# Performance work log

Hardware: AMD Instinct MI355X
Metric: run time of the kernel (lower is better)

The kernel has to match this reference:

```python
import jax, jax.numpy as jnp
import numpy as np

NEG_SLOPE = 0.1  # LeakyReLU alpha from __init__
EPS = 1e-5


def setup_inputs() -> dict:
    key = jax.random.key(0)
    k1, k2, k3, k4, k5 = jax.random.split(key, 5)
    N, E, DIN, DOUT = 10000, 160000, 1024, 1024
    x = jax.random.normal(k1, (N, DIN), dtype=jnp.float32)
    W = jax.random.normal(k2, (DIN, DOUT), dtype=jnp.float32) * 0.02  # xavier-ish gain
    a = jax.random.normal(k3, (1, 2 * DOUT), dtype=jnp.float32) * 0.02
    src = jax.random.randint(k4, (E,), 0, N, dtype=jnp.int64)  # edge rows i
    dst = jax.random.randint(k5, (E,), 0, N, dtype=jnp.int64)  # edge cols j
    return {"x": x, "W": W, "a": a, "src": src, "dst": dst}


def reference(x, W, a, src, dst):
    N = x.shape[0]
    d = W.shape[1]
    h = x @ W                                   # [N, d]
    # a @ cat(h_src, h_dst)^T == (h @ a_l)[src] + (h @ a_r)[dst]
    a_l, a_r = a[0, :d], a[0, d:]
    al = h @ a_l                                # [N]
    ar = h @ a_r                                # [N]
    e = jnp.exp(-jax.nn.leaky_relu(al[src] + ar[dst], negative_slope=NEG_SLOPE))  # [E]
    # sparse rowsum: A @ ones  ->  segment_sum of e over rows
    rowsum = jax.ops.segment_sum(e, src, num_segments=N)          # [N]
    # sparse aggregate: A @ h  (dropout = identity in eval mode)
    h_prime = jax.ops.segment_sum(e[:, None] * h[dst], src, num_segments=N)  # [N, d]
    h_prime = h_prime / (rowsum[:, None] + EPS)
    return jax.nn.elu(h_prime)  # concat=True branch
```

## Files before the change

### kernel.cpp

```cpp
#include <hip/hip_runtime.h>
#include <hip/hip_bf16.h>
#include <stdint.h>
#include <math.h>

#define DK 1024
#define DN 1024
#define CAP 64

typedef __attribute__((ext_vector_type(8))) short bf16x8;
typedef __attribute__((ext_vector_type(4))) float f32x4;

__device__ __forceinline__ unsigned short f2bf(float f) {
  union { float f; uint32_t u; } v; v.f = f;
  uint32_t r = v.u + 0x7FFFu + ((v.u >> 16) & 1u);
  return (unsigned short)(r >> 16);
}
__device__ __forceinline__ float bf2f(unsigned short b) {
  union { uint32_t u; float f; } v; v.u = ((uint32_t)b) << 16; return v.f;
}

__device__ __forceinline__ void gload_lds16(const void* g, void* l) {
  __builtin_amdgcn_global_load_lds((const __attribute__((address_space(1))) unsigned int*)g,
                                   (__attribute__((address_space(3))) unsigned int*)l,
                                   16, 0, 0);
}

__device__ __forceinline__ void block_reduce2(float& pl, float& pr) {
#pragma unroll
  for (int off = 32; off >= 1; off >>= 1) {
    pl += __shfl_down(pl, off);
    pr += __shfl_down(pr, off);
  }
  __shared__ float sl[4], sr[4];
  int w = threadIdx.x >> 6, lane = threadIdx.x & 63;
  if (lane == 0) { sl[w] = pl; sr[w] = pr; }
  __syncthreads();
  if (threadIdx.x == 0) {
    pl = sl[0] + sl[1] + sl[2] + sl[3];
    pr = sr[0] + sr[1] + sr[2] + sr[3];
  }
}

__global__ __launch_bounds__(256) void wvec_kernel(const float* __restrict__ W,
                                                   const float* __restrict__ a,
                                                   float* __restrict__ wl,
                                                   float* __restrict__ wr,
                                                   int* __restrict__ cnt, int M) {
  int idx = blockIdx.x * 256 + threadIdx.x;
  if (idx < M) cnt[idx] = 0;
  int k = blockIdx.x;
  int tid = threadIdx.x;
  float4 wv = ((const float4*)(W + (size_t)k * DN))[tid];
  float4 l4 = ((const float4*)a)[tid];
  float4 r4 = ((const float4*)(a + DN))[tid];
  float pl = wv.x * l4.x + wv.y * l4.y + wv.z * l4.z + wv.w * l4.w;
  float pr = wv.x * r4.x + wv.y * r4.y + wv.z * r4.z + wv.w * r4.w;
  block_reduce2(pl, pr);
  if (tid == 0) { wl[k] = pl; wr[k] = pr; }
}

__global__ __launch_bounds__(256) void prep_kernel(const float* __restrict__ x,
                                                   unsigned short* __restrict__ xb,
                                                   const float* __restrict__ W,
                                                   unsigned short* __restrict__ Wt,
                                                   const float* __restrict__ wl,
                                                   const float* __restrict__ wr,
                                                   float* __restrict__ al,
                                                   float* __restrict__ ar,
                                                   int M) {
  if ((int)blockIdx.x < M) {
    int row = blockIdx.x;
    int tid = threadIdx.x;
    float4 v = ((const float4*)(x + (size_t)row * DK))[tid];
    ushort4 o;
    o.x = f2bf(v.x); o.y = f2bf(v.y); o.z = f2bf(v.z); o.w = f2bf(v.w);
    ((ushort4*)(xb + (size_t)row * DK))[tid] = o;
    float4 l4 = ((const float4*)wl)[tid];
    float4 r4 = ((const float4*)wr)[tid];
    float pl = v.x * l4.x + v.y * l4.y + v.z * l4.z + v.w * l4.w;
    float pr = v.x * r4.x + v.y * r4.y + v.z * r4.z + v.w * r4.w;
    block_reduce2(pl, pr);
    if (tid == 0) { al[row] = pl; ar[row] = pr; }
  } else {
    __shared__ float t[32][33];
    int bid = blockIdx.x - M;
    int tx = threadIdx.x & 31, ty = threadIdx.x >> 5;
    int bk = (bid & 31) * 32, bn = (bid >> 5) * 32;
#pragma unroll
    for (int rr = 0; rr < 4; ++rr) {
      int row = ty + rr * 8;
      t[row][tx] = W[(size_t)(bk + row) * DN + bn + tx];
    }
    __syncthreads();
#pragma unroll
    for (int rr = 0; rr < 4; ++rr) {
      int row = ty + rr * 8;
      Wt[(size_t)(bn + row) * DK + bk + tx] = f2bf(t[tx][row]);
    }
  }
}

__global__ __launch_bounds__(256) void gemm_kernel(const unsigned short* __restrict__ A,
                                                   const unsigned short* __restrict__ Bt,
                                                   unsigned short* __restrict__ Hb,
                                                   int M) {
  __shared__ unsigned short As[128 * 32];
  __shared__ unsigned short Bs[128 * 32];
  const int tid = threadIdx.x;
  const int w = tid >> 6, lane = tid & 63;
  const int r = lane & 15, q = lane >> 4;
  const int m0 = blockIdx.x * 128, n0 = blockIdx.y * 128;
  const int wr = (w >> 1) * 64, wc = (w & 1) * 64;

  const int c0 = w * 64 + lane;
  const int rowA0 = c0 >> 2, g0 = c0 & 3;
  const int rowA1 = rowA0 + 64;
  int gr0 = m0 + rowA0; if (gr0 >= M) gr0 = M - 1;
  int gr1 = m0 + rowA1; if (gr1 >= M) gr1 = M - 1;
  const unsigned short* gA0 = A + (size_t)gr0 * DK + g0 * 8;
  const unsigned short* gA1 = A + (size_t)gr1 * DK + g0 * 8;
  const unsigned short* gB0 = Bt + (size_t)(n0 + rowA0) * DK + g0 * 8;
  const unsigned short* gB1 = Bt + (size_t)(n0 + rowA1) * DK + g0 * 8;
  unsigned short* lA0 = As + w * 512;
  unsigned short* lA1 = As + 2048 + w * 512;
  unsigned short* lB0 = Bs + w * 512;
  unsigned short* lB1 = Bs + 2048 + w * 512;

  const f32x4 zero = {0.f, 0.f, 0.f, 0.f};
  f32x4 acc[4][4];
#pragma unroll
  for (int i = 0; i < 4; ++i)
#pragma unroll
    for (int j = 0; j < 4; ++j) acc[i][j] = zero;

  for (int k0 = 0; k0 < DK; k0 += 32) {
    gload_lds16(gA0, lA0);
    gload_lds16(gA1, lA1);
    gload_lds16(gB0, lB0);
    gload_lds16(gB1, lB1);
    gA0 += 32; gA1 += 32; gB0 += 32; gB1 += 32;
    __syncthreads();

    bf16x8 af[4], bfr[4];
#pragma unroll
    for (int i = 0; i < 4; ++i)
      af[i] = *(const bf16x8*)&As[(wr + i * 16 + r) * 32 + q * 8];
#pragma unroll
    for (int j = 0; j < 4; ++j)
      bfr[j] = *(const bf16x8*)&Bs[(wc + j * 16 + r) * 32 + q * 8];
#pragma unroll
    for (int i = 0; i < 4; ++i)
#pragma unroll
      for (int j = 0; j < 4; ++j)
        acc[i][j] = __builtin_amdgcn_mfma_f32_16x16x32_bf16(af[i], bfr[j], acc[i][j], 0, 0, 0);
    __syncthreads();
  }

#pragma unroll
  for (int i = 0; i < 4; ++i) {
#pragma unroll
    for (int reg = 0; reg < 4; ++reg) {
      int m = m0 + wr + i * 16 + q * 4 + reg;
      if (m < M) {
#pragma unroll
        for (int j = 0; j < 4; ++j) {
          int n = n0 + wc + j * 16 + r;
          Hb[(size_t)m * DN + n] = f2bf(acc[i][j][reg]);
        }
      }
    }
  }
}

__global__ __launch_bounds__(256) void edge_kernel(const int* __restrict__ src,
                                                   const int* __restrict__ dst,
                                                   const float* __restrict__ al,
                                                   const float* __restrict__ ar,
                                                   int* __restrict__ cnt,
                                                   int* __restrict__ bdst,
                                                   float* __restrict__ be, int E) {
  int i = blockIdx.x * 256 + threadIdx.x;
  if (i < E) {
    int s = src[i], d = dst[i];
    float v = al[s] + ar[d];
    float lr = v > 0.f ? v : 0.1f * v;
    float e = expf(-lr);
    int pos = atomicAdd(&cnt[s], 1);
    if (pos < CAP) {
      bdst[(s << 6) + pos] = d;
      be[(s << 6) + pos] = e;
    }
  }
}

__global__ __launch_bounds__(256) void aggregate_kernel(const int* __restrict__ cnt,
                                                        const int* __restrict__ bdst,
                                                        const float* __restrict__ be,
                                                        const unsigned short* __restrict__ Hb,
                                                        float* __restrict__ out, int M) {
  int row = blockIdx.x;
  int tid = threadIdx.x;
  int n = cnt[row]; if (n > CAP) n = CAP;
  int base = row << 6;
  size_t coff = (size_t)tid * 4;
  float a0 = 0.f, a1 = 0.f, a2 = 0.f, a3 = 0.f, rs = 0.f;
  int p = 0;
  for (; p + 8 <= n; p += 8) {
    int4 da = *(const int4*)(bdst + base + p);
    int4 db = *(const int4*)(bdst + base + p + 4);
    float4 ea = *(const float4*)(be + base + p);
    float4 eb = *(const float4*)(be + base + p + 4);
    ushort4 h0 = *(const ushort4*)&Hb[(size_t)da.x * DN + coff];
    ushort4 h1 = *(const ushort4*)&Hb[(size_t)da.y * DN + coff];
    ushort4 h2 = *(const ushort4*)&Hb[(size_t)da.z * DN + coff];
    ushort4 h3 = *(const ushort4*)&Hb[(size_t)da.w * DN + coff];
    ushort4 h4 = *(const ushort4*)&Hb[(size_t)db.x * DN + coff];
    ushort4 h5 = *(const ushort4*)&Hb[(size_t)db.y * DN + coff];
    ushort4 h6 = *(const ushort4*)&Hb[(size_t)db.z * DN + coff];
    ushort4 h7 = *(const ushort4*)&Hb[(size_t)db.w * DN + coff];
    rs += ((ea.x + ea.y) + (ea.z + ea.w)) + ((eb.x + eb.y) + (eb.z + eb.w));
    a0 += ea.x * bf2f(h0.x) + ea.y * bf2f(h1.x) + ea.z * bf2f(h2.x) + ea.w * bf2f(h3.x)
        + eb.x * bf2f(h4.x) + eb.y * bf2f(h5.x) + eb.z * bf2f(h6.x) + eb.w * bf2f(h7.x);
    a1 += ea.x * bf2f(h0.y) + ea.y * bf2f(h1.y) + ea.z * bf2f(h2.y) + ea.w * bf2f(h3.y)
        + eb.x * bf2f(h4.y) + eb.y * bf2f(h5.y) + eb.z * bf2f(h6.y) + eb.w * bf2f(h7.y);
    a2 += ea.x * bf2f(h0.z) + ea.y * bf2f(h1.z) + ea.z * bf2f(h2.z) + ea.w * bf2f(h3.z)
        + eb.x * bf2f(h4.z) + eb.y * bf2f(h5.z) + eb.z * bf2f(h6.z) + eb.w * bf2f(h7.z);
    a3 += ea.x * bf2f(h0.w) + ea.y * bf2f(h1.w) + ea.z * bf2f(h2.w) + ea.w * bf2f(h3.w)
        + eb.x * bf2f(h4.w) + eb.y * bf2f(h5.w) + eb.z * bf2f(h6.w) + eb.w * bf2f(h7.w);
  }
  for (; p + 4 <= n; p += 4) {
    int4 d4 = *(const int4*)(bdst + base + p);
    float4 e4 = *(const float4*)(be + base + p);
    ushort4 h0 = *(const ushort4*)&Hb[(size_t)d4.x * DN + coff];
    ushort4 h1 = *(const ushort4*)&Hb[(size_t)d4.y * DN + coff];
    ushort4 h2 = *(const ushort4*)&Hb[(size_t)d4.z * DN + coff];
    ushort4 h3 = *(const ushort4*)&Hb[(size_t)d4.w * DN + coff];
    rs += (e4.x + e4.y) + (e4.z + e4.w);
    a0 += e4.x * bf2f(h0.x) + e4.y * bf2f(h1.x) + e4.z * bf2f(h2.x) + e4.w * bf2f(h3.x);
    a1 += e4.x * bf2f(h0.y) + e4.y * bf2f(h1.y) + e4.z * bf2f(h2.y) + e4.w * bf2f(h3.y);
    a2 += e4.x * bf2f(h0.z) + e4.y * bf2f(h1.z) + e4.z * bf2f(h2.z) + e4.w * bf2f(h3.z);
    a3 += e4.x * bf2f(h0.w) + e4.y * bf2f(h1.w) + e4.z * bf2f(h2.w) + e4.w * bf2f(h3.w);
  }
  for (; p < n; ++p) {
    int d = bdst[base + p];
    float e = be[base + p];
    rs += e;
    ushort4 hv = *(const ushort4*)&Hb[(size_t)d * DN + coff];
    a0 += e * bf2f(hv.x);
    a1 += e * bf2f(hv.y);
    a2 += e * bf2f(hv.z);
    a3 += e * bf2f(hv.w);
  }
  float inv = 1.f / (rs + 1e-5f);
  float4 o; float v;
  v = a0 * inv; o.x = v > 0.f ? v : (expf(v) - 1.f);
  v = a1 * inv; o.y = v > 0.f ? v : (expf(v) - 1.f);
  v = a2 * inv; o.z = v > 0.f ? v : (expf(v) - 1.f);
  v = a3 * inv; o.w = v > 0.f ? v : (expf(v) - 1.f);
  ((float4*)(out + (size_t)row * DN))[tid] = o;
}

extern "C" void kernel_launch(void* const* d_in, const int* in_sizes, int n_in,
                              void* d_out, int out_size, void* d_ws, size_t ws_size,
                              hipStream_t stream) {
  const float* x = (const float*)d_in[0];
  const float* W = (const float*)d_in[1];
  const float* a = (const float*)d_in[2];
  const int* src = (const int*)d_in[3];
  const int* dst = (const int*)d_in[4];
  float* out = (float*)d_out;
  const int M = in_sizes[0] / DK;
  const int E = in_sizes[3];

  size_t off = 0;
  auto alloc = [&](size_t bytes) -> void* {
    void* p = (char*)d_ws + off;
    off += (bytes + 255) & ~(size_t)255;
    return p;
  };
  unsigned short* xb   = (unsigned short*)alloc((size_t)M * DK * 2);
  unsigned short* Wt   = (unsigned short*)alloc((size_t)DK * DN * 2);
  unsigned short* Hb   = (unsigned short*)alloc((size_t)M * DN * 2);
  float*          al   = (float*)alloc((size_t)M * 4);
  float*          ar   = (float*)alloc((size_t)M * 4);
  float*          wl   = (float*)alloc((size_t)DK * 4);
  float*          wr   = (float*)alloc((size_t)DK * 4);
  int*            cnt  = (int*)alloc((size_t)M * 4);
  int*            bdst = (int*)alloc((size_t)M * CAP * 4);
  float*          be   = (float*)alloc((size_t)M * CAP * 4);

  wvec_kernel<<<DK, 256, 0, stream>>>(W, a, wl, wr, cnt, M);
  prep_kernel<<<M + (DK / 32) * (DN / 32), 256, 0, stream>>>(x, xb, W, Wt, wl, wr, al, ar, M);
  gemm_kernel<<<dim3((M + 127) / 128, DN / 128), 256, 0, stream>>>(xb, Wt, Hb, M);
  edge_kernel<<<(E + 255) / 256, 256, 0, stream>>>(src, dst, al, ar, cnt, bdst, be, E);
  aggregate_kernel<<<M, 256, 0, stream>>>(cnt, bdst, be, Hb, out, M);
}
```

Before: 194.7 us.

## Shrink GEMM M-tile to 64 rows and XOR-swizzle LDS tiles

Changes the GEMM block tile from 128x128 to 64x128, so each wave computes a 32x64 sub-tile and twice as many blocks launch. This gives more blocks for the 256 CUs (the 10000x1024 output previously made only ~632 blocks). It also applies an XOR swizzle on the 16-byte chunk index in the LDS tiles to reduce bank conflicts on fragment reads. The cost is less data reuse per block, with the B tile loaded twice as often from global memory.

Result: slower. 200.7 us (+3.1%).

```diff
diff --git a/kernel.cpp b/kernel.cpp
--- a/kernel.cpp
+++ b/kernel.cpp
@@ -104,52 +104,55 @@
                                                    const unsigned short* __restrict__ Bt,
                                                    unsigned short* __restrict__ Hb,
                                                    int M) {
-  __shared__ unsigned short As[128 * 32];
+  __shared__ unsigned short As[64 * 32];
   __shared__ unsigned short Bs[128 * 32];
   const int tid = threadIdx.x;
   const int w = tid >> 6, lane = tid & 63;
   const int r = lane & 15, q = lane >> 4;
-  const int m0 = blockIdx.x * 128, n0 = blockIdx.y * 128;
-  const int wr = (w >> 1) * 64, wc = (w & 1) * 64;
-
-  const int c0 = w * 64 + lane;
-  const int rowA0 = c0 >> 2, g0 = c0 & 3;
-  const int rowA1 = rowA0 + 64;
-  int gr0 = m0 + rowA0; if (gr0 >= M) gr0 = M - 1;
-  int gr1 = m0 + rowA1; if (gr1 >= M) gr1 = M - 1;
-  const unsigned short* gA0 = A + (size_t)gr0 * DK + g0 * 8;
-  const unsigned short* gA1 = A + (size_t)gr1 * DK + g0 * 8;
-  const unsigned short* gB0 = Bt + (size_t)(n0 + rowA0) * DK + g0 * 8;
-  const unsigned short* gB1 = Bt + (size_t)(n0 + rowA1) * DK + g0 * 8;
-  unsigned short* lA0 = As + w * 512;
-  unsigned short* lA1 = As + 2048 + w * 512;
-  unsigned short* lB0 = Bs + w * 512;
-  unsigned short* lB1 = Bs + 2048 + w * 512;
+  const int m0 = blockIdx.x * 64, n0 = blockIdx.y * 128;
+  const int wr = (w >> 1) * 32, wc = (w & 1) * 64;
+
+  const int cA = w * 64 + lane;
+  const int rA = cA >> 2, gA = (cA & 3) ^ ((rA >> 1) & 3);
+  int grA = m0 + rA; if (grA >= M) grA = M - 1;
+  const unsigned short* gpA = A + (size_t)grA * DK + gA * 8;
+  unsigned short* lpA = As + w * 512;
+
+  const int cB0 = w * 64 + lane, cB1 = cB0 + 256;
+  const int rB0 = cB0 >> 2, gB0i = (cB0 & 3) ^ ((rB0 >> 1) & 3);
+  const int rB1 = cB1 >> 2, gB1i = (cB1 & 3) ^ ((rB1 >> 1) & 3);
+  const unsigned short* gpB0 = Bt + (size_t)(n0 + rB0) * DK + gB0i * 8;
+  const unsigned short* gpB1 = Bt + (size_t)(n0 + rB1) * DK + gB1i * 8;
+  unsigned short* lpB0 = Bs + w * 512;
+  unsigned short* lpB1 = Bs + 2048 + w * 512;
 
   const f32x4 zero = {0.f, 0.f, 0.f, 0.f};
-  f32x4 acc[4][4];
-#pragma unroll
-  for (int i = 0; i < 4; ++i)
+  f32x4 acc[2][4];
+#pragma unroll
+  for (int i = 0; i < 2; ++i)
 #pragma unroll
     for (int j = 0; j < 4; ++j) acc[i][j] = zero;
 
   for (int k0 = 0; k0 < DK; k0 += 32) {
-    gload_lds16(gA0, lA0);
-    gload_lds16(gA1, lA1);
-    gload_lds16(gB0, lB0);
-    gload_lds16(gB1, lB1);
-    gA0 += 32; gA1 += 32; gB0 += 32; gB1 += 32;
+    gload_lds16(gpA, lpA);
+    gload_lds16(gpB0, lpB0);
+    gload_lds16(gpB1, lpB1);
+    gpA += 32; gpB0 += 32; gpB1 += 32;
     __syncthreads();
 
-    bf16x8 af[4], bfr[4];
-#pragma unroll
-    for (int i = 0; i < 4; ++i)
-      af[i] = *(const bf16x8*)&As[(wr + i * 16 + r) * 32 + q * 8];
-#pragma unroll
-    for (int j = 0; j < 4; ++j)
-      bfr[j] = *(const bf16x8*)&Bs[(wc + j * 16 + r) * 32 + q * 8];
-#pragma unroll
-    for (int i = 0; i < 4; ++i)
+    bf16x8 af[2], bfr[4];
+#pragma unroll
+    for (int i = 0; i < 2; ++i) {
+      int rr = wr + i * 16 + r;
+      af[i] = *(const bf16x8*)&As[rr * 32 + ((q ^ ((rr >> 1) & 3)) * 8)];
+    }
+#pragma unroll
+    for (int j = 0; j < 4; ++j) {
+      int rn = wc + j * 16 + r;
+      bfr[j] = *(const bf16x8*)&Bs[rn * 32 + ((q ^ ((rn >> 1) & 3)) * 8)];
+    }
+#pragma unroll
+    for (int i = 0; i < 2; ++i)
 #pragma unroll
       for (int j = 0; j < 4; ++j)
         acc[i][j] = __builtin_amdgcn_mfma_f32_16x16x32_bf16(af[i], bfr[j], acc[i][j], 0, 0, 0);
@@ -157,7 +160,7 @@
   }
 
 #pragma unroll
-  for (int i = 0; i < 4; ++i) {
+  for (int i = 0; i < 2; ++i) {
 #pragma unroll
     for (int reg = 0; reg < 4; ++reg) {
       int m = m0 + wr + i * 16 + q * 4 + reg;
@@ -291,7 +294,7 @@
 
   wvec_kernel<<<DK, 256, 0, stream>>>(W, a, wl, wr, cnt, M);
   prep_kernel<<<M + (DK / 32) * (DN / 32), 256, 0, stream>>>(x, xb, W, Wt, wl, wr, al, ar, M);
-  gemm_kernel<<<dim3((M + 127) / 128, DN / 128), 256, 0, stream>>>(xb, Wt, Hb, M);
+  gemm_kernel<<<dim3((M + 63) / 64, DN / 128), 256, 0, stream>>>(xb, Wt, Hb, M);
   edge_kernel<<<(E + 255) / 256, 256, 0, stream>>>(src, dst, al, ar, cnt, bdst, be, E);
   aggregate_kernel<<<M, 256, 0, stream>>>(cnt, bdst, be, Hb, out, M);
 }
```

## Split aggregate over column chunks with one wave per row

Applied to the files above, without the earlier changes.

The aggregate kernel now gives each wave one row and one 128-column chunk, and the grid covers 8 column chunks by row groups of 4. Chunks are ordered outermost, so concurrently running blocks all touch the same 128-column slice of H. This aims to keep the gathered H slice resident in L2/MALL instead of streaming full 2KB rows. In exchange each lane issues narrower 4-byte gathers, the 8-way unrolled loop is dropped, and the bdst/be index lists are re-read once per chunk.

New measurement: 200.7 us. 3.1% more time.

```diff
diff --git a/kernel.cpp b/kernel.cpp
--- a/kernel.cpp
+++ b/kernel.cpp
@@ -6,6 +6,7 @@
 #define DK 1024
 #define DN 1024
 #define CAP 64
+#define NCHUNK 8
 
 typedef __attribute__((ext_vector_type(8))) short bf16x8;
 typedef __attribute__((ext_vector_type(4))) float f32x4;
@@ -197,67 +198,43 @@
                                                         const int* __restrict__ bdst,
                                                         const float* __restrict__ be,
                                                         const unsigned short* __restrict__ Hb,
-                                                        float* __restrict__ out, int M) {
-  int row = blockIdx.x;
-  int tid = threadIdx.x;
+                                                        float* __restrict__ out,
+                                                        int M, int nrowgrp) {
+  int chunk = blockIdx.x / nrowgrp;
+  int rowgrp = blockIdx.x - chunk * nrowgrp;
+  int wv = threadIdx.x >> 6, lane = threadIdx.x & 63;
+  int row = rowgrp * 4 + wv;
+  if (row >= M) return;
   int n = cnt[row]; if (n > CAP) n = CAP;
   int base = row << 6;
-  size_t coff = (size_t)tid * 4;
-  float a0 = 0.f, a1 = 0.f, a2 = 0.f, a3 = 0.f, rs = 0.f;
+  int col = chunk * 128 + lane * 2;
+  const unsigned short* hb = Hb + col;
+  float a0 = 0.f, a1 = 0.f, rs = 0.f;
   int p = 0;
-  for (; p + 8 <= n; p += 8) {
-    int4 da = *(const int4*)(bdst + base + p);
-    int4 db = *(const int4*)(bdst + base + p + 4);
-    float4 ea = *(const float4*)(be + base + p);
-    float4 eb = *(const float4*)(be + base + p + 4);
-    ushort4 h0 = *(const ushort4*)&Hb[(size_t)da.x * DN + coff];
-    ushort4 h1 = *(const ushort4*)&Hb[(size_t)da.y * DN + coff];
-    ushort4 h2 = *(const ushort4*)&Hb[(size_t)da.z * DN + coff];
-    ushort4 h3 = *(const ushort4*)&Hb[(size_t)da.w * DN + coff];
-    ushort4 h4 = *(const ushort4*)&Hb[(size_t)db.x * DN + coff];
-    ushort4 h5 = *(const ushort4*)&Hb[(size_t)db.y * DN + coff];
-    ushort4 h6 = *(const ushort4*)&Hb[(size_t)db.z * DN + coff];
-    ushort4 h7 = *(const ushort4*)&Hb[(size_t)db.w * DN + coff];
-    rs += ((ea.x + ea.y) + (ea.z + ea.w)) + ((eb.x + eb.y) + (eb.z + eb.w));
-    a0 += ea.x * bf2f(h0.x) + ea.y * bf2f(h1.x) + ea.z * bf2f(h2.x) + ea.w * bf2f(h3.x)
-        + eb.x * bf2f(h4.x) + eb.y * bf2f(h5.x) + eb.z * bf2f(h6.x) + eb.w * bf2f(h7.x);
-    a1 += ea.x * bf2f(h0.y) + ea.y * bf2f(h1.y) + ea.z * bf2f(h2.y) + ea.w * bf2f(h3.y)
-        + eb.x * bf2f(h4.y) + eb.y * bf2f(h5.y) + eb.z * bf2f(h6.y) + eb.w * bf2f(h7.y);
-    a2 += ea.x * bf2f(h0.z) + ea.y * bf2f(h1.z) + ea.z * bf2f(h2.z) + ea.w * bf2f(h3.z)
-        + eb.x * bf2f(h4.z) + eb.y * bf2f(h5.z) + eb.z * bf2f(h6.z) + eb.w * bf2f(h7.z);
-    a3 += ea.x * bf2f(h0.w) + ea.y * bf2f(h1.w) + ea.z * bf2f(h2.w) + ea.w * bf2f(h3.w)
-        + eb.x * bf2f(h4.w) + eb.y * bf2f(h5.w) + eb.z * bf2f(h6.w) + eb.w * bf2f(h7.w);
-  }
   for (; p + 4 <= n; p += 4) {
     int4 d4 = *(const int4*)(bdst + base + p);
     float4 e4 = *(const float4*)(be + base + p);
-    ushort4 h0 = *(const ushort4*)&Hb[(size_t)d4.x * DN + coff];
-    ushort4 h1 = *(const ushort4*)&Hb[(size_t)d4.y * DN + coff];
-    ushort4 h2 = *(const ushort4*)&Hb[(size_t)d4.z * DN + coff];
-    ushort4 h3 = *(const ushort4*)&Hb[(size_t)d4.w * DN + coff];
+    ushort2 h0 = *(const ushort2*)&hb[(size_t)d4.x * DN];
+    ushort2 h1 = *(const ushort2*)&hb[(size_t)d4.y * DN];
+    ushort2 h2 = *(const ushort2*)&hb[(size_t)d4.z * DN];
+    ushort2 h3 = *(const ushort2*)&hb[(size_t)d4.w * DN];
     rs += (e4.x + e4.y) + (e4.z + e4.w);
     a0 += e4.x * bf2f(h0.x) + e4.y * bf2f(h1.x) + e4.z * bf2f(h2.x) + e4.w * bf2f(h3.x);
     a1 += e4.x * bf2f(h0.y) + e4.y * bf2f(h1.y) + e4.z * bf2f(h2.y) + e4.w * bf2f(h3.y);
-    a2 += e4.x * bf2f(h0.z) + e4.y * bf2f(h1.z) + e4.z * bf2f(h2.z) + e4.w * bf2f(h3.z);
-    a3 += e4.x * bf2f(h0.w) + e4.y * bf2f(h1.w) + e4.z * bf2f(h2.w) + e4.w * bf2f(h3.w);
   }
   for (; p < n; ++p) {
     int d = bdst[base + p];
     float e = be[base + p];
     rs += e;
-    ushort4 hv = *(const ushort4*)&Hb[(size_t)d * DN + coff];
+    ushort2 hv = *(const ushort2*)&hb[(size_t)d * DN];
     a0 += e * bf2f(hv.x);
     a1 += e * bf2f(hv.y);
-    a2 += e * bf2f(hv.z);
-    a3 += e * bf2f(hv.w);
   }
   float inv = 1.f / (rs + 1e-5f);
-  float4 o; float v;
+  float2 o; float v;
   v = a0 * inv; o.x = v > 0.f ? v : (expf(v) - 1.f);
   v = a1 * inv; o.y = v > 0.f ? v : (expf(v) - 1.f);
-  v = a2 * inv; o.z = v > 0.f ? v : (expf(v) - 1.f);
-  v = a3 * inv; o.w = v > 0.f ? v : (expf(v) - 1.f);
-  ((float4*)(out + (size_t)row * DN))[tid] = o;
+  *(float2*)(out + (size_t)row * DN + col) = o;
 }
 
 extern "C" void kernel_launch(void* const* d_in, const int* in_sizes, int n_in,
@@ -293,5 +270,6 @@
   prep_kernel<<<M + (DK / 32) * (DN / 32), 256, 0, stream>>>(x, xb, W, Wt, wl, wr, al, ar, M);
   gemm_kernel<<<dim3((M + 127) / 128, DN / 128), 256, 0, stream>>>(xb, Wt, Hb, M);
   edge_kernel<<<(E + 255) / 256, 256, 0, stream>>>(src, dst, al, ar, cnt, bdst, be, E);
-  aggregate_kernel<<<M, 256, 0, stream>>>(cnt, bdst, be, Hb, out, M);
-}
+  int nrowgrp = (M + 3) / 4;
+  aggregate_kernel<<<NCHUNK * nrowgrp, 256, 0, stream>>>(cnt, bdst, be, Hb, out, M, nrowgrp);
+}
```
